# Performance work log

Measured on AMD Instinct MI355X. Metric: run time of the kernel, lower is better.

## Reference

```python
import jax, jax.numpy as jnp
import numpy as np

B, N, CIN, K, HID = 16, 4096, 64, 64, 128
RATIO, RADIUS = 0.25, 0.2
S = int(N * RATIO)  # 1024 sampled centers per cloud


def setup_inputs() -> dict:
    key = jax.random.key(0)
    k1, k2, k3, k4 = jax.random.split(key, 4)
    x = jax.random.normal(k1, (B * N, CIN), jnp.float32)
    pos = jax.random.uniform(k2, (B * N, 3), jnp.float32)  # unit cube
    batch = jnp.repeat(jnp.arange(B, dtype=jnp.int32), N)  # sorted cloud ids
    W1 = jax.random.normal(k3, (CIN + 3, HID), jnp.float32) / np.sqrt(CIN + 3)
    b1 = jnp.zeros((HID,), jnp.float32)
    W2 = jax.random.normal(k4, (HID, HID), jnp.float32) / np.sqrt(HID)
    b2 = jnp.zeros((HID,), jnp.float32)
    return {"x": x, "pos": pos, "batch": batch, "W1": W1, "b1": b1, "W2": W2, "b2": b2}


def _fps(pos_b):
    """Farthest point sampling on one cloud [N,3] -> S int32 indices (start=0, deterministic)."""
    def step(carry, _):
        min_d, last = carry
        d = jnp.sum((pos_b - pos_b[last]) ** 2, axis=-1)  # [N]
        min_d = jnp.minimum(min_d, d)
        nxt = jnp.argmax(min_d).astype(jnp.int32)
        return (min_d, nxt), last
    init = (jnp.full((N,), jnp.inf, pos_b.dtype), jnp.int32(0))
    _, idx = jax.lax.scan(step, init, None, length=S)
    return idx  # [S]


def _forward(x, pos, W1, b1, W2, b2):
    xb = x.reshape(B, N, CIN)
    pb = pos.reshape(B, N, 3)
    idx = jax.vmap(_fps)(pb)  # [B,S]
    centers = jnp.take_along_axis(pb, idx[:, :, None], axis=1)  # [B,S,3]
    # ball query: squared dists centers->all points of same cloud
    d2 = jnp.sum((centers[:, :, None, :] - pb[:, None, :, :]) ** 2, axis=-1)  # [B,S,N]
    masked = jnp.where(d2 <= RADIUS * RADIUS, d2, jnp.inf)
    negv, nbr = jax.lax.top_k(-masked, K)  # K nearest within radius; [B,S,K]
    valid = negv > -jnp.inf  # [B,S,K]
    gather = jax.vmap(lambda a, i: a[i])
    x_j = gather(xb, nbr)  # [B,S,K,CIN]
    p_j = gather(pb, nbr)  # [B,S,K,3]
    rel = p_j - centers[:, :, None, :]
    h = jnp.concatenate([x_j, rel], axis=-1)  # [B,S,K,CIN+3]
    h = jax.nn.relu(h @ W1 + b1)
    h = jax.nn.relu(h @ W2 + b2)  # local_nn message
    h = jnp.where(valid[..., None], h, -jnp.inf)
    out = jnp.max(h, axis=2)  # max-aggregation over neighbors -> [B,S,HID]
    return out.reshape(B * S, HID), centers.reshape(B * S, 3)


def reference(x, pos, batch, W1, b1, W2, b2):
    out, pos_out = _forward(x, pos, W1, b1, W2, b2)
    batch_out = jnp.repeat(jnp.arange(B, dtype=jnp.int32), S)
    return out, pos_out, batch_out
```

## Files before the change

kernel.cpp:

```cpp
#include <hip/hip_runtime.h>
#include <cstdint>
#include <cstddef>

#define BB   16
#define NN   4096
#define CINN 64
#define KKK  64
#define HIDD 128
#define SSS  1024
#define MAXC 320
#define CHS  512

typedef __attribute__((ext_vector_type(8))) short short8;
typedef __attribute__((ext_vector_type(4))) float f32x4;
typedef unsigned long long u64;

__device__ __forceinline__ float d2_exact(float ax, float ay, float az,
                                          float bx, float by, float bz) {
  float dx = __fsub_rn(ax, bx);
  float dy = __fsub_rn(ay, by);
  float dz = __fsub_rn(az, bz);
  return __fadd_rn(__fadd_rn(__fmul_rn(dx, dx), __fmul_rn(dy, dy)), __fmul_rn(dz, dz));
}

__device__ __forceinline__ unsigned short f2bf(float f) {
  unsigned u = __float_as_uint(f);
  return (unsigned short)((u + 0x7fffu + ((u >> 16) & 1u)) >> 16);
}

__device__ __forceinline__ void fps_role(int chunk, int bid, int tid,
                                         const float* __restrict__ pos,
                                         int* __restrict__ fps_idx,
                                         float* __restrict__ md_ws,
                                         int* __restrict__ last_ws,
                                         float* __restrict__ pos_out,
                                         float* __restrict__ batch_out,
                                         char* smem) {
  __builtin_amdgcn_s_setprio(3);
  float* px = (float*)smem;
  float* py = px + NN;
  float* pz = py + NN;
  u64* slots = (u64*)(pz + NN);
  int* sel = (int*)(slots + 8);
  const float* pb = pos + (size_t)bid * NN * 3;
  for (int i = tid; i < NN; i += 256) {
    px[i] = pb[3 * i + 0];
    py[i] = pb[3 * i + 1];
    pz[i] = pb[3 * i + 2];
  }
  if (chunk == 0) {
    #pragma unroll
    for (int kk = 0; kk < 4; ++kk)
      batch_out[bid * SSS + kk * 256 + tid] = (float)bid;
  }
  __syncthreads();

  float qx[16], qy[16], qz[16], md[16];
  #pragma unroll
  for (int j = 0; j < 16; ++j) {
    const int i = j * 256 + tid;
    qx[j] = px[i]; qy[j] = py[i]; qz[j] = pz[i];
    asm volatile("" : "+v"(qx[j]), "+v"(qy[j]), "+v"(qz[j]));
    md[j] = __builtin_inff();
  }
  int last, tb;
  const int cbase = chunk * CHS;
  const int te = cbase + CHS;
  if (chunk == 0) {
    last = 0; tb = 1;
    if (tid == 0) {
      fps_idx[bid * SSS] = 0;
      pos_out[(size_t)bid * SSS * 3 + 0] = px[0];
      pos_out[(size_t)bid * SSS * 3 + 1] = py[0];
      pos_out[(size_t)bid * SSS * 3 + 2] = pz[0];
    }
  } else {
    #pragma unroll
    for (int j = 0; j < 16; ++j) md[j] = md_ws[bid * 4096 + j * 256 + tid];
    last = last_ws[bid]; tb = cbase;
  }

  for (int t = tb; t < te; ++t) {
    const float lx = px[last], ly = py[last], lz = pz[last];
    float bv = -1.f;
    int bj = 0;
    #pragma unroll
    for (int j = 0; j < 16; ++j) {
      const float d = d2_exact(qx[j], qy[j], qz[j], lx, ly, lz);
      md[j] = fminf(md[j], d);
      if (md[j] > bv) { bv = md[j]; bj = j; }
    }
    unsigned klo = ~(unsigned)(bj * 256 + tid);
    unsigned khi = __float_as_uint(bv);
#define FPS_DPP_STAGE(CTRL, RMASK)                                                            \
    {                                                                                          \
      unsigned slo = (unsigned)__builtin_amdgcn_update_dpp(0, (int)klo, CTRL, RMASK, 0xf, true); \
      unsigned shi = (unsigned)__builtin_amdgcn_update_dpp(0, (int)khi, CTRL, RMASK, 0xf, true); \
      if ((((u64)shi << 32) | slo) > (((u64)khi << 32) | klo)) { khi = shi; klo = slo; }       \
    }
    FPS_DPP_STAGE(0x111, 0xf)
    FPS_DPP_STAGE(0x112, 0xf)
    FPS_DPP_STAGE(0x114, 0xf)
    FPS_DPP_STAGE(0x118, 0xf)
    FPS_DPP_STAGE(0x142, 0xa)
    FPS_DPP_STAGE(0x143, 0xc)
#undef FPS_DPP_STAGE
    u64* sl = slots + (t & 1) * 4;
    if ((tid & 63) == 63) sl[tid >> 6] = ((u64)khi << 32) | klo;
    __syncthreads();
    u64 mm = sl[0];
    #pragma unroll
    for (int w = 1; w < 4; ++w) mm = sl[w] > mm ? sl[w] : mm;
    last = (int)(~(unsigned)(mm & 0xffffffffull));
    if (tid == 0) sel[t - cbase] = last;
  }

  __syncthreads();
  for (int e = tid; e < CHS; e += 256) {
    const int t2 = cbase + e;
    if (t2 == 0) continue;
    const int idx = sel[e];
    fps_idx[bid * SSS + t2] = idx;
    pos_out[((size_t)bid * SSS + t2) * 3 + 0] = px[idx];
    pos_out[((size_t)bid * SSS + t2) * 3 + 1] = py[idx];
    pos_out[((size_t)bid * SSS + t2) * 3 + 2] = pz[idx];
  }
  if (chunk == 0) {
    #pragma unroll
    for (int j = 0; j < 16; ++j) md_ws[bid * 4096 + j * 256 + tid] = md[j];
    if (tid == 0) last_ws[bid] = last;
  }
}

__device__ __forceinline__ void y1_role(int j, int tid,
                                        const float* __restrict__ x,
                                        const float* __restrict__ W1,
                                        unsigned short* __restrict__ y1,
                                        char* smem) {
  float* sW = (float*)smem;
  float* sx = (float*)(smem + 32768);
  const int cloud = ((j >> 12) << 3) | (j & 7);
  const int local = (j >> 3) & 511;
  const int p0 = cloud * NN + local * 8;
  for (int e = tid; e < CINN * HIDD; e += 256) sW[e] = W1[e];
  for (int e = tid; e < 8 * CINN; e += 256) sx[e] = x[(size_t)p0 * CINN + e];
  __syncthreads();
  const int h = tid & 127;
  const int pg = (tid >> 7) * 4;
  float a0 = 0.f, a1 = 0.f, a2 = 0.f, a3 = 0.f;
  for (int c = 0; c < CINN; ++c) {
    const float w = sW[c * HIDD + h];
    a0 = fmaf(sx[(pg + 0) * CINN + c], w, a0);
    a1 = fmaf(sx[(pg + 1) * CINN + c], w, a1);
    a2 = fmaf(sx[(pg + 2) * CINN + c], w, a2);
    a3 = fmaf(sx[(pg + 3) * CINN + c], w, a3);
  }
  y1[(size_t)(p0 + pg + 0) * HIDD + h] = f2bf(a0);
  y1[(size_t)(p0 + pg + 1) * HIDD + h] = f2bf(a1);
  y1[(size_t)(p0 + pg + 2) * HIDD + h] = f2bf(a2);
  y1[(size_t)(p0 + pg + 3) * HIDD + h] = f2bf(a3);
}

__device__ __forceinline__ void bq_role(int cc, int i, int tid,
                                        const float* __restrict__ pos,
                                        const int* __restrict__ fps_idx,
                                        int* __restrict__ nbr,
                                        int* __restrict__ cnt,
                                        char* smem) {
  const int b = i >> 6;
  const int t0 = cc * CHS + (i & 63) * 8;
  const int gbase = b * SSS + t0;
  float* cd = (float*)smem;
  int*   ci = (int*)(smem + 10240);
  int*   ctr = (int*)(smem + 20480);
  int*   scn = ctr + 8;
  float* cctr = (float*)(scn + 8);

  const float* pb = pos + (size_t)b * NN * 3;
  if (tid < 8) { ctr[tid] = 0; scn[tid] = 0; }
  if (tid < 8) {
    const int cp = fps_idx[gbase + tid];
    cctr[tid * 3 + 0] = pb[cp * 3 + 0];
    cctr[tid * 3 + 1] = pb[cp * 3 + 1];
    cctr[tid * 3 + 2] = pb[cp * 3 + 2];
  }
  __syncthreads();
  float cx[8], cy[8], cz[8];
  #pragma unroll
  for (int c = 0; c < 8; ++c) {
    cx[c] = cctr[c * 3 + 0]; cy[c] = cctr[c * 3 + 1]; cz[c] = cctr[c * 3 + 2];
  }
  #pragma unroll 4
  for (int s2 = 0; s2 < 16; ++s2) {
    const int p = s2 * 256 + tid;
    const float x = pb[3 * p + 0], y = pb[3 * p + 1], z = pb[3 * p + 2];
    #pragma unroll
    for (int c = 0; c < 8; ++c) {
      const float d2 = d2_exact(x, y, z, cx[c], cy[c], cz[c]);
      if (d2 <= 0.04f) {
        const int slot = atomicAdd(&ctr[c], 1);
        if (slot < MAXC) { cd[c * MAXC + slot] = d2; ci[c * MAXC + slot] = p; }
      }
    }
  }
  __syncthreads();
  #pragma unroll 1
  for (int c = 0; c < 8; ++c) {
    const int C = min(ctr[c], MAXC);
    for (int j = tid; j < C; j += 256) {
      const float dj = cd[c * MAXC + j];
      const int ij = ci[c * MAXC + j];
      int rank = 0;
      for (int m = 0; m < C; ++m) {
        const float dm = cd[c * MAXC + m];
        const int im = ci[c * MAXC + m];
        rank += (dm < dj || (dm == dj && im < ij)) ? 1 : 0;
      }
      if (rank < KKK) nbr[(size_t)(gbase + c) * KKK + atomicAdd(&scn[c], 1)] = ij;
    }
  }
  __syncthreads();
  if (tid < 8) cnt[gbase + tid] = scn[tid];
}

__device__ __forceinline__ void mlp_role(int cc, int m, int tid,
                                         const float* __restrict__ pos,
                                         const unsigned short* __restrict__ y1,
                                         const float* __restrict__ W1,
                                         const float* __restrict__ b1,
                                         const unsigned short* __restrict__ W2t,
                                         const float* __restrict__ b2,
                                         const int* __restrict__ fps_idx,
                                         const int* __restrict__ nbr,
                                         const int* __restrict__ cnt,
                                         float* __restrict__ out,
                                         char* smem) {
  const int b = ((m >> 11) << 3) | (m & 7);
  const int loc = (m >> 3) & 255;
  const int g0 = b * SSS + cc * CHS + loc * 2;
  char* Hb = smem;
  float* s_ctr = (float*)(smem + 32768);
  int* s_M = (int*)(smem + 32800);
  int* s_pidx = (int*)(smem + 32832);
  float* s_rel = (float*)(smem + 33344);

  const int wv = tid >> 6, ln = tid & 63;
  const int mw = wv >> 1, nw = wv & 1;
  const int lr = ln & 15, lg = ln >> 4;

  short8 bfr[4][4];
  #pragma unroll
  for (int ks = 0; ks < 4; ++ks)
    #pragma unroll
    for (int ni = 0; ni < 4; ++ni)
      bfr[ks][ni] = *(const short8*)(W2t + (size_t)(nw * 64 + ni * 16 + lr) * HIDD + ks * 32 + lg * 8);

  if (tid < 2) {
    s_M[tid] = min(cnt[g0 + tid], KKK);
    const int cp = fps_idx[g0 + tid];
    s_ctr[tid * 3 + 0] = pos[((size_t)b * NN + cp) * 3 + 0];
    s_ctr[tid * 3 + 1] = pos[((size_t)b * NN + cp) * 3 + 1];
    s_ctr[tid * 3 + 2] = pos[((size_t)b * NN + cp) * 3 + 2];
  }
  __syncthreads();

  if (tid < 128) {
    const int ci = tid >> 6, k = tid & 63;
    int p = -1;
    float rx = 0.f, ry = 0.f, rz = 0.f;
    if (k < s_M[ci]) {
      p = nbr[(size_t)(g0 + ci) * KKK + k];
      rx = pos[((size_t)b * NN + p) * 3 + 0] - s_ctr[ci * 3 + 0];
      ry = pos[((size_t)b * NN + p) * 3 + 1] - s_ctr[ci * 3 + 1];
      rz = pos[((size_t)b * NN + p) * 3 + 2] - s_ctr[ci * 3 + 2];
    }
    s_pidx[tid] = p;
    s_rel[tid * 3 + 0] = rx; s_rel[tid * 3 + 1] = ry; s_rel[tid * 3 + 2] = rz;
  }
  __syncthreads();

  const float2 b1v = *(const float2*)(b1 + ln * 2);
  const float2 wav = *(const float2*)(W1 + 64 * HIDD + ln * 2);
  const float2 wbv = *(const float2*)(W1 + 65 * HIDD + ln * 2);
  const float2 wcv = *(const float2*)(W1 + 66 * HIDD + ln * 2);
  const int rbase = wv * 32;
  #pragma unroll
  for (int half = 0; half < 2; ++half) {
    unsigned yreg[16];
    #pragma unroll
    for (int rr = 0; rr < 16; ++rr) {
      const int p = s_pidx[rbase + half * 16 + rr];
      const int pa = p < 0 ? 0 : p;
      yreg[rr] = *(const unsigned*)(y1 + ((size_t)(b * NN + pa)) * HIDD + ln * 2);
    }
    #pragma unroll
    for (int rr = 0; rr < 16; ++rr) {
      const int r = rbase + half * 16 + rr;
      const int p = s_pidx[r];
      unsigned val = 0u;
      if (p >= 0) {
        const float rx = s_rel[r * 3 + 0], ry = s_rel[r * 3 + 1], rz = s_rel[r * 3 + 2];
        const float y0 = __uint_as_float(yreg[rr] << 16);
        const float y1f = __uint_as_float(yreg[rr] & 0xffff0000u);
        const float v0 = fmaxf(y0 + b1v.x + rx * wav.x + ry * wbv.x + rz * wcv.x, 0.f);
        const float v1 = fmaxf(y1f + b1v.y + rx * wav.y + ry * wbv.y + rz * wcv.y, 0.f);
        val = (unsigned)f2bf(v0) | ((unsigned)f2bf(v1) << 16);
      }
      *(unsigned*)(Hb + r * 256 + ((ln * 4) ^ ((r & 7) << 4))) = val;
    }
  }
  __syncthreads();

  f32x4 zero = {0.f, 0.f, 0.f, 0.f};
  f32x4 acc[4][4];
  #pragma unroll
  for (int mi = 0; mi < 4; ++mi)
    #pragma unroll
    for (int ni = 0; ni < 4; ++ni) acc[mi][ni] = zero;

  #pragma unroll
  for (int ks = 0; ks < 4; ++ks) {
    short8 af[4];
    #pragma unroll
    for (int mi = 0; mi < 4; ++mi) {
      const int row = mw * 64 + mi * 16 + lr;
      af[mi] = *(const short8*)(Hb + row * 256 + ((ks * 64 + lg * 16) ^ ((row & 7) << 4)));
    }
    #pragma unroll
    for (int mi = 0; mi < 4; ++mi)
      #pragma unroll
      for (int ni = 0; ni < 4; ++ni)
        acc[mi][ni] = __builtin_amdgcn_mfma_f32_16x16x32_bf16(af[mi], bfr[ks][ni], acc[mi][ni], 0, 0, 0);
  }

  const int cId = g0 + mw;
  const int Mc = s_M[mw];
  #pragma unroll
  for (int ni = 0; ni < 4; ++ni) {
    const float b2v = b2[nw * 64 + ni * 16 + lr];
    float cm = 0.f;
    #pragma unroll
    for (int mi = 0; mi < 4; ++mi)
      #pragma unroll
      for (int rr = 0; rr < 4; ++rr) {
        const int k = mi * 16 + lg * 4 + rr;
        const float v = fmaxf(acc[mi][ni][rr] + b2v, 0.f);
        cm = fmaxf(cm, k < Mc ? v : 0.f);
      }
    cm = fmaxf(cm, __shfl_xor(cm, 16, 64));
    cm = fmaxf(cm, __shfl_xor(cm, 32, 64));
    if (ln < 16) out[(size_t)cId * HIDD + nw * 64 + ni * 16 + lr] = cm;
  }
}

__global__ __launch_bounds__(256) void k_phase0(const float* __restrict__ x,
                                                const float* __restrict__ pos,
                                                const float* __restrict__ W1,
                                                const float* __restrict__ W2,
                                                unsigned short* __restrict__ W2t,
                                                int* __restrict__ fps_idx,
                                                unsigned short* __restrict__ y1,
                                                float* __restrict__ md_ws,
                                                int* __restrict__ last_ws,
                                                float* __restrict__ pos_out,
                                                float* __restrict__ batch_out) {
  __shared__ __align__(16) char smem[51264];
  const int bid = blockIdx.x, tid = threadIdx.x;
  if (bid < BB) {
    fps_role(0, bid, tid, pos, fps_idx, md_ws, last_ws, pos_out, batch_out, smem);
  } else if (bid < 16 + 8192) {
    y1_role(bid - 16, tid, x, W1, y1, smem);
  } else {
    for (int e = tid; e < HIDD * HIDD; e += 256) {
      const int n = e >> 7, hh = e & 127;
      W2t[e] = f2bf(W2[hh * HIDD + n]);
    }
  }
}

__global__ __launch_bounds__(256) void k_phase1(const float* __restrict__ pos,
                                                int* __restrict__ fps_idx,
                                                int* __restrict__ cnt,
                                                int* __restrict__ nbr,
                                                float* __restrict__ md_ws,
                                                int* __restrict__ last_ws,
                                                float* __restrict__ pos_out,
                                                float* __restrict__ batch_out) {
  __shared__ __align__(16) char smem[51264];
  const int bid = blockIdx.x, tid = threadIdx.x;
  if (bid < BB) {
    fps_role(1, bid, tid, pos, fps_idx, md_ws, last_ws, pos_out, batch_out, smem);
  } else {
    bq_role(0, bid - 16, tid, pos, fps_idx, nbr, cnt, smem);
  }
}

__global__ __launch_bounds__(256) void k_phase2(const float* __restrict__ pos,
                                                const int* __restrict__ fps_idx,
                                                int* __restrict__ nbr,
                                                int* __restrict__ cnt) {
  __shared__ __align__(16) char smem[20736];
  bq_role(1, blockIdx.x, threadIdx.x, pos, fps_idx, nbr, cnt, smem);
}

__global__ __launch_bounds__(256, 4) void k_phase3(const float* __restrict__ pos,
                                                   const unsigned short* __restrict__ y1,
                                                   const float* __restrict__ W1,
                                                   const float* __restrict__ b1,
                                                   const unsigned short* __restrict__ W2t,
                                                   const float* __restrict__ b2,
                                                   const int* __restrict__ fps_idx,
                                                   const int* __restrict__ nbr,
                                                   const int* __restrict__ cnt,
                                                   float* __restrict__ out) {
  __shared__ __align__(16) char smem[34944];
  const int bid = blockIdx.x;
  mlp_role(bid >> 12, bid & 4095, threadIdx.x, pos, y1, W1, b1, W2t, b2,
           fps_idx, nbr, cnt, out, smem);
}

extern "C" void kernel_launch(void* const* d_in, const int* in_sizes, int n_in,
                              void* d_out, int out_size, void* d_ws, size_t ws_size,
                              hipStream_t stream) {
  const float* x   = (const float*)d_in[0];
  const float* pos = (const float*)d_in[1];
  const float* W1  = (const float*)d_in[3];
  const float* b1  = (const float*)d_in[4];
  const float* W2  = (const float*)d_in[5];
  const float* b2  = (const float*)d_in[6];

  float* out       = (float*)d_out;
  float* pos_out   = out + (size_t)BB * SSS * HIDD;
  float* batch_out = pos_out + (size_t)BB * SSS * 3;

  int* fps_idx        = (int*)d_ws;
  int* cnt            = (int*)((char*)d_ws + 65536);
  unsigned short* W2t = (unsigned short*)((char*)d_ws + 131072);
  int* last_ws        = (int*)((char*)d_ws + 163840);
  int* nbr            = (int*)((char*)d_ws + 262144);
  unsigned short* y1  = (unsigned short*)((char*)d_ws + 262144 + 4194304);
  float* md_ws        = (float*)((char*)d_ws + 262144 + 4194304 + 33554432);

  k_phase0<<<16 + 8192 + 1, 256, 0, stream>>>(x, pos, W1, W2, W2t, fps_idx, y1,
                                              md_ws, last_ws, pos_out, batch_out);
  k_phase1<<<16 + 1024, 256, 0, stream>>>(pos, fps_idx, cnt, nbr,
                                          md_ws, last_ws, pos_out, batch_out);
  k_phase2<<<1024, 256, 0, stream>>>(pos, fps_idx, nbr, cnt);
  k_phase3<<<8192, 256, 0, stream>>>(pos, y1, W1, b1, W2t, b2,
                                     fps_idx, nbr, cnt, out);
}
```

Measured before the change: 857.9 us.

## Pipeline FPS, ball query and MLP across four chunks in fused launches

```diff
diff --git a/kernel.cpp b/kernel.cpp
--- a/kernel.cpp
+++ b/kernel.cpp
@@ -9,7 +9,8 @@
 #define HIDD 128
 #define SSS  1024
 #define MAXC 320
-#define CHS  512
+#define NCH  4
+#define CHS  256
 
 typedef __attribute__((ext_vector_type(8))) short short8;
 typedef __attribute__((ext_vector_type(4))) float f32x4;
@@ -125,7 +126,7 @@
     pos_out[((size_t)bid * SSS + t2) * 3 + 1] = py[idx];
     pos_out[((size_t)bid * SSS + t2) * 3 + 2] = pz[idx];
   }
-  if (chunk == 0) {
+  if (chunk != NCH - 1) {
     #pragma unroll
     for (int j = 0; j < 16; ++j) md_ws[bid * 4096 + j * 256 + tid] = md[j];
     if (tid == 0) last_ws[bid] = last;
@@ -167,8 +168,8 @@
                                         int* __restrict__ nbr,
                                         int* __restrict__ cnt,
                                         char* smem) {
-  const int b = i >> 6;
-  const int t0 = cc * CHS + (i & 63) * 8;
+  const int b = i >> 5;
+  const int t0 = cc * CHS + (i & 31) * 8;
   const int gbase = b * SSS + t0;
   float* cd = (float*)smem;
   int*   ci = (int*)(smem + 10240);
@@ -235,8 +236,8 @@
                                          const int* __restrict__ cnt,
                                          float* __restrict__ out,
                                          char* smem) {
-  const int b = ((m >> 11) << 3) | (m & 7);
-  const int loc = (m >> 3) & 255;
+  const int b = ((m >> 10) << 3) | (m & 7);
+  const int loc = (m >> 3) & 127;
   const int g0 = b * SSS + cc * CHS + loc * 2;
   char* Hb = smem;
   float* s_ctr = (float*)(smem + 32768);
@@ -395,27 +396,55 @@
   }
 }
 
-__global__ __launch_bounds__(256) void k_phase2(const float* __restrict__ pos,
-                                                const int* __restrict__ fps_idx,
+__global__ __launch_bounds__(256) void k_phaseM(int c,
+                                                const float* __restrict__ pos,
+                                                const unsigned short* __restrict__ y1,
+                                                const float* __restrict__ W1,
+                                                const float* __restrict__ b1,
+                                                const unsigned short* __restrict__ W2t,
+                                                const float* __restrict__ b2,
+                                                int* __restrict__ fps_idx,
+                                                int* __restrict__ cnt,
                                                 int* __restrict__ nbr,
-                                                int* __restrict__ cnt) {
+                                                float* __restrict__ md_ws,
+                                                int* __restrict__ last_ws,
+                                                float* __restrict__ out,
+                                                float* __restrict__ pos_out,
+                                                float* __restrict__ batch_out) {
+  __shared__ __align__(16) char smem[51264];
+  const int bid = blockIdx.x, tid = threadIdx.x;
+  if (bid < BB) {
+    fps_role(c, bid, tid, pos, fps_idx, md_ws, last_ws, pos_out, batch_out, smem);
+  } else if (bid < 16 + 512) {
+    bq_role(c - 1, bid - 16, tid, pos, fps_idx, nbr, cnt, smem);
+  } else {
+    mlp_role(c - 2, bid - (16 + 512), tid, pos, y1, W1, b1, W2t, b2,
+             fps_idx, nbr, cnt, out, smem);
+  }
+}
+
+__global__ __launch_bounds__(256) void k_bq3(const float* __restrict__ pos,
+                                             const int* __restrict__ fps_idx,
+                                             int* __restrict__ nbr,
+                                             int* __restrict__ cnt) {
   __shared__ __align__(16) char smem[20736];
-  bq_role(1, blockIdx.x, threadIdx.x, pos, fps_idx, nbr, cnt, smem);
-}
-
-__global__ __launch_bounds__(256, 4) void k_phase3(const float* __restrict__ pos,
-                                                   const unsigned short* __restrict__ y1,
-                                                   const float* __restrict__ W1,
-                                                   const float* __restrict__ b1,
-                                                   const unsigned short* __restrict__ W2t,
-                                                   const float* __restrict__ b2,
-                                                   const int* __restrict__ fps_idx,
-                                                   const int* __restrict__ nbr,
-                                                   const int* __restrict__ cnt,
-                                                   float* __restrict__ out) {
+  bq_role(NCH - 1, blockIdx.x, threadIdx.x, pos, fps_idx, nbr, cnt, smem);
+}
+
+__global__ __launch_bounds__(256, 4) void k_mlptail(const float* __restrict__ pos,
+                                                    const unsigned short* __restrict__ y1,
+                                                    const float* __restrict__ W1,
+                                                    const float* __restrict__ b1,
+                                                    const unsigned short* __restrict__ W2t,
+                                                    const float* __restrict__ b2,
+                                                    const int* __restrict__ fps_idx,
+                                                    const int* __restrict__ nbr,
+                                                    const int* __restrict__ cnt,
+                                                    float* __restrict__ out) {
   __shared__ __align__(16) char smem[34944];
   const int bid = blockIdx.x;
-  mlp_role(bid >> 12, bid & 4095, threadIdx.x, pos, y1, W1, b1, W2t, b2,
+  const int cc = (bid < 2048) ? (NCH - 2) : (NCH - 1);
+  mlp_role(cc, bid & 2047, threadIdx.x, pos, y1, W1, b1, W2t, b2,
            fps_idx, nbr, cnt, out, smem);
 }
 
@@ -443,9 +472,15 @@
 
   k_phase0<<<16 + 8192 + 1, 256, 0, stream>>>(x, pos, W1, W2, W2t, fps_idx, y1,
                                               md_ws, last_ws, pos_out, batch_out);
-  k_phase1<<<16 + 1024, 256, 0, stream>>>(pos, fps_idx, cnt, nbr,
-                                          md_ws, last_ws, pos_out, batch_out);
-  k_phase2<<<1024, 256, 0, stream>>>(pos, fps_idx, nbr, cnt);
-  k_phase3<<<8192, 256, 0, stream>>>(pos, y1, W1, b1, W2t, b2,
-                                     fps_idx, nbr, cnt, out);
-}
+  k_phase1<<<16 + 512, 256, 0, stream>>>(pos, fps_idx, cnt, nbr,
+                                         md_ws, last_ws, pos_out, batch_out);
+  k_phaseM<<<16 + 512 + 2048, 256, 0, stream>>>(2, pos, y1, W1, b1, W2t, b2,
+                                                fps_idx, cnt, nbr, md_ws, last_ws,
+                                                out, pos_out, batch_out);
+  k_phaseM<<<16 + 512 + 2048, 256, 0, stream>>>(3, pos, y1, W1, b1, W2t, b2,
+                                                fps_idx, cnt, nbr, md_ws, last_ws,
+                                                out, pos_out, batch_out);
+  k_bq3<<<512, 256, 0, stream>>>(pos, fps_idx, nbr, cnt);
+  k_mlptail<<<4096, 256, 0, stream>>>(pos, y1, W1, b1, W2t, b2,
+                                      fps_idx, nbr, cnt, out);
+}
```

New measurement: 909.8 us. +6.1%, slower.
